# Optimization experiments

Hardware: AMD Instinct MI355X
Metric: run time of the kernel (lower is better)

The kernel has to match this reference:

```python
import jax, jax.numpy as jnp
import numpy as np

EPS = 1e-12


def _sq_dists(x, y):
    # x: [B, N1, 3], y: [B, N2, 3] -> squared pairwise distances [B, N1, N2]
    x2 = jnp.sum(x * x, axis=-1)            # [B, N1]
    y2 = jnp.sum(y * y, axis=-1)            # [B, N2]
    xy = jnp.einsum('bnd,bmd->bnm', x, y)   # [B, N1, N2]
    d = x2[:, :, None] + y2[:, None, :] - 2.0 * xy
    return jnp.maximum(d, 0.0)


def setup_inputs() -> dict:
    key = jax.random.key(0)
    k1, k2 = jax.random.split(key)
    xyz1 = jax.random.normal(k1, (8, 8192, 3), dtype=jnp.float32)
    xyz2 = jax.random.normal(k2, (8, 8192, 3), dtype=jnp.float32)
    return {"xyz1": xyz1, "xyz2": xyz2}


def reference(xyz1, xyz2):
    d = _sq_dists(xyz1, xyz2)                       # [B, N1, N2]
    dist1 = jnp.min(d, axis=2)                      # nearest in xyz2 for each xyz1 point
    dist2 = jnp.min(d, axis=1)                      # nearest in xyz1 for each xyz2 point
    dist1 = jnp.sqrt(jnp.maximum(dist1, EPS))
    dist2 = jnp.sqrt(jnp.maximum(dist2, EPS))
    per_batch = (jnp.mean(dist1, axis=1) + jnp.mean(dist2, axis=1)) / 2.0  # [B]
    return jnp.mean(per_batch)
```

## Files before the change

kernel.cpp:

```cpp
#include <hip/hip_runtime.h>
#include <math.h>


#define NPTS   8192
#define NB     8
#define NPC    (NB * NPTS)
#define BLOCK  512
#define CHUNK  1024
#define COLS   NPTS
#define TOTALQ (2 * NPC)
#define EPSV   1e-12f
#define FXSCALE 67108864.0

typedef _Float16 v8h  __attribute__((ext_vector_type(8)));
typedef float    v16f __attribute__((ext_vector_type(16)));

__global__ __launch_bounds__(256) void chamfer_prep(
    const float* __restrict__ xyz1, const float* __restrict__ xyz2,
    v8h* __restrict__ form, unsigned long long* __restrict__ counter)
{
    const int gid = blockIdx.x * 256 + threadIdx.x;
    if (gid == 0) counter[0] = 0ULL;
    const float* __restrict__ src = (gid < NPC) ? xyz1 : xyz2;
    const int i = (gid < NPC) ? gid : gid - NPC;
    float x = src[3 * i], y = src[3 * i + 1], z = src[3 * i + 2];
    _Float16 xh = (_Float16)x, yh = (_Float16)y, zh = (_Float16)z;
    float xf = (float)xh, yf = (float)yh, zf = (float)zh;
    float n = fmaf(xf, xf, fmaf(yf, yf, zf * zf));
    v8h bv = {};
    bv[0] = xh; bv[1] = yh; bv[2] = zh;
    bv[3] = (_Float16)n; bv[4] = (_Float16)1.0f;
    form[gid] = bv;
}

#define MFMA(va, vb) __builtin_amdgcn_mfma_f32_32x32x16_f16((va), (vb), vzero, 0, 0, 0)

__global__ __launch_bounds__(BLOCK, 4) void chamfer_mfma_min(
    const v8h* __restrict__ form, unsigned long long* __restrict__ counter)
{
    const int bid = blockIdx.x;
    const int rb  = bid & 31;
    const int b   = (bid >> 5) & 7;
    const int dir = (bid >> 8) & 1;

    const v8h* __restrict__ qf = form + (size_t)dir * NPC + (size_t)b * NPTS;
    const v8h* __restrict__ tf = form + (size_t)(1 - dir) * NPC + (size_t)b * NPTS;

    const int tid  = threadIdx.x;
    const int lane = tid & 63;
    const int w    = tid >> 6;
    const int c31  = lane & 31;
    const int rowbase = rb * 256;

    v8h a0 = {};
    if (lane < 32) {
        const _Float16 m2 = (_Float16)(-2.0f);
        v8h f = qf[rowbase + w * 32 + lane];
        a0[0] = m2 * f[0]; a0[1] = m2 * f[1]; a0[2] = m2 * f[2];
        a0[3] = (_Float16)1.0f; a0[4] = f[3];
    }

    float rm0[16];
#pragma unroll
    for (int r = 0; r < 16; ++r) rm0[r] = 3.4e38f;

    __shared__ v8h bsh[CHUNK];
    const v16f vzero = {};

    for (int ch = 0; ch < COLS / CHUNK; ++ch) {
        __syncthreads();
        const v8h* __restrict__ g = tf + ch * CHUNK;
#pragma unroll
        for (int k = 0; k < CHUNK / BLOCK; ++k)
            bsh[k * BLOCK + tid] = g[k * BLOCK + tid];
        __syncthreads();

#pragma unroll
        for (int cc = 0; cc < CHUNK / 64; ++cc) {
            const v8h b0 = bsh[cc * 64 + c31];
            const v8h b1 = bsh[cc * 64 + 32 + c31];
            __builtin_amdgcn_s_setprio(1);
            v16f p = MFMA(a0, b0);
            v16f q = MFMA(a0, b1);
            __builtin_amdgcn_s_setprio(0);
#pragma unroll
            for (int r = 0; r < 16; ++r)
                rm0[r] = fminf(fminf(rm0[r], p[r]), q[r]);
        }
    }

    float acc = 0.0f;
#pragma unroll
    for (int r = 0; r < 16; ++r) {
        float v = rm0[r];
        v = fminf(v, __shfl_xor(v, 1));
        v = fminf(v, __shfl_xor(v, 2));
        v = fminf(v, __shfl_xor(v, 4));
        v = fminf(v, __shfl_xor(v, 8));
        v = fminf(v, __shfl_xor(v, 16));
        if ((lane & 31) == 0)
            acc += sqrtf(fmaxf(fmaxf(v, 0.0f), EPSV));
    }
    acc += __shfl_xor(acc, 32);

    __syncthreads();
    float* red = (float*)bsh;
    if (lane == 0) red[w] = acc;
    __syncthreads();
    if (tid == 0) {
        float s = red[0] + red[1] + red[2] + red[3]
                + red[4] + red[5] + red[6] + red[7];
        unsigned long long fx = (unsigned long long)((double)s * FXSCALE + 0.5);
        atomicAdd(counter, fx);
    }
}

__global__ void chamfer_finalize(
    const unsigned long long* __restrict__ counter, float* __restrict__ out)
{
    out[0] = (float)((double)counter[0] * (1.0 / FXSCALE) / (double)TOTALQ);
}

extern "C" void kernel_launch(void* const* d_in, const int* in_sizes, int n_in,
                              void* d_out, int out_size, void* d_ws, size_t ws_size,
                              hipStream_t stream) {
    const float* xyz1 = (const float*)d_in[0];
    const float* xyz2 = (const float*)d_in[1];
    float* out = (float*)d_out;

    v8h* formbuf = (v8h*)d_ws;
    unsigned long long* counter = (unsigned long long*)(formbuf + TOTALQ);

    chamfer_prep<<<TOTALQ / 256, 256, 0, stream>>>(xyz1, xyz2, formbuf, counter);
    chamfer_mfma_min<<<2 * NB * 32, BLOCK, 0, stream>>>(formbuf, counter);
    chamfer_finalize<<<1, 1, 0, stream>>>(counter, out);
}
```

Baseline: 46.56 us.

## Register-block two query tiles per wave and use unsigned integer min

Each wave now holds two A fragments (64 query rows) and reuses every LDS-loaded B fragment for four MFMAs instead of two. The block shrinks to 256 threads so the grid and row coverage stay the same. The running minima become unsigned integer mins on the bit-cast floats, which avoids float min canonicalization. This halves the LDS reads per MFMA but doubles accumulator registers and halves the number of waves per CU. Negative distances are treated as very large under the integer ordering, so near-zero results can differ slightly from the reference.

```diff
diff --git a/kernel.cpp b/kernel.cpp
--- a/kernel.cpp
+++ b/kernel.cpp
@@ -5,7 +5,7 @@
 #define NPTS   8192
 #define NB     8
 #define NPC    (NB * NPTS)
-#define BLOCK  512
+#define BLOCK  256
 #define CHUNK  1024
 #define COLS   NPTS
 #define TOTALQ (2 * NPC)
@@ -35,6 +35,10 @@
 
 #define MFMA(va, vb) __builtin_amdgcn_mfma_f32_32x32x16_f16((va), (vb), vzero, 0, 0, 0)
 
+__device__ __forceinline__ unsigned umin2(unsigned a, unsigned b) {
+    return a < b ? a : b;
+}
+
 __global__ __launch_bounds__(BLOCK, 4) void chamfer_mfma_min(
     const v8h* __restrict__ form, unsigned long long* __restrict__ counter)
 {
@@ -52,17 +56,20 @@
     const int c31  = lane & 31;
     const int rowbase = rb * 256;
 
-    v8h a0 = {};
+    v8h a0 = {}, a1 = {};
     if (lane < 32) {
         const _Float16 m2 = (_Float16)(-2.0f);
-        v8h f = qf[rowbase + w * 32 + lane];
+        v8h f = qf[rowbase + w * 64 + lane];
         a0[0] = m2 * f[0]; a0[1] = m2 * f[1]; a0[2] = m2 * f[2];
         a0[3] = (_Float16)1.0f; a0[4] = f[3];
+        f = qf[rowbase + w * 64 + 32 + lane];
+        a1[0] = m2 * f[0]; a1[1] = m2 * f[1]; a1[2] = m2 * f[2];
+        a1[3] = (_Float16)1.0f; a1[4] = f[3];
     }
 
-    float rm0[16];
+    unsigned rm0[16], rm1[16];
 #pragma unroll
-    for (int r = 0; r < 16; ++r) rm0[r] = 3.4e38f;
+    for (int r = 0; r < 16; ++r) { rm0[r] = 0x7F7F7F7FU; rm1[r] = 0x7F7F7F7FU; }
 
     __shared__ v8h bsh[CHUNK];
     const v16f vzero = {};
@@ -80,26 +87,38 @@
             const v8h b0 = bsh[cc * 64 + c31];
             const v8h b1 = bsh[cc * 64 + 32 + c31];
             __builtin_amdgcn_s_setprio(1);
-            v16f p = MFMA(a0, b0);
-            v16f q = MFMA(a0, b1);
+            v16f p0 = MFMA(a0, b0);
+            v16f q0 = MFMA(a0, b1);
+            v16f p1 = MFMA(a1, b0);
+            v16f q1 = MFMA(a1, b1);
             __builtin_amdgcn_s_setprio(0);
 #pragma unroll
             for (int r = 0; r < 16; ++r)
-                rm0[r] = fminf(fminf(rm0[r], p[r]), q[r]);
+                rm0[r] = umin2(rm0[r], umin2(__builtin_bit_cast(unsigned, p0[r]),
+                                             __builtin_bit_cast(unsigned, q0[r])));
+#pragma unroll
+            for (int r = 0; r < 16; ++r)
+                rm1[r] = umin2(rm1[r], umin2(__builtin_bit_cast(unsigned, p1[r]),
+                                             __builtin_bit_cast(unsigned, q1[r])));
         }
     }
 
     float acc = 0.0f;
 #pragma unroll
-    for (int r = 0; r < 16; ++r) {
-        float v = rm0[r];
-        v = fminf(v, __shfl_xor(v, 1));
-        v = fminf(v, __shfl_xor(v, 2));
-        v = fminf(v, __shfl_xor(v, 4));
-        v = fminf(v, __shfl_xor(v, 8));
-        v = fminf(v, __shfl_xor(v, 16));
-        if ((lane & 31) == 0)
-            acc += sqrtf(fmaxf(fmaxf(v, 0.0f), EPSV));
+    for (int s = 0; s < 2; ++s) {
+#pragma unroll
+        for (int r = 0; r < 16; ++r) {
+            unsigned u = s ? rm1[r] : rm0[r];
+            u = umin2(u, __shfl_xor(u, 1));
+            u = umin2(u, __shfl_xor(u, 2));
+            u = umin2(u, __shfl_xor(u, 4));
+            u = umin2(u, __shfl_xor(u, 8));
+            u = umin2(u, __shfl_xor(u, 16));
+            if ((lane & 31) == 0) {
+                float v = __builtin_bit_cast(float, u);
+                acc += sqrtf(fmaxf(fmaxf(v, 0.0f), EPSV));
+            }
+        }
     }
     acc += __shfl_xor(acc, 32);
 
@@ -108,8 +127,7 @@
     if (lane == 0) red[w] = acc;
     __syncthreads();
     if (tid == 0) {
-        float s = red[0] + red[1] + red[2] + red[3]
-                + red[4] + red[5] + red[6] + red[7];
+        float s = red[0] + red[1] + red[2] + red[3];
         unsigned long long fx = (unsigned long long)((double)s * FXSCALE + 0.5);
         atomicAdd(counter, fx);
     }
```

After: 45.57 us, median of 3. 1.02x faster.
